# Kernel optimization log

Measured on AMD Instinct MI355X. Metric: run time of the kernel, lower is better.

## Reference

```python
import jax, jax.numpy as jnp
import numpy as np

# irreps kept in the output (sorted): 0e (dim 1), 1o (dim 3), 2e (dim 5)
IRS = (("0e", 1), ("1o", 3), ("2e", 5))
# multiplicity of each irrep in the reduced symmetric tensor product basis per order
MULS = {1: {"0e": 1, "1o": 1, "2e": 1},
        2: {"0e": 2, "1o": 2, "2e": 3},
        3: {"0e": 4, "1o": 6, "2e": 8}}
N, C, D, S, CORR = 1024, 128, 9, 10, 3  # nodes, channels, irreps dim (0e+1o+2e), species, correlation


def setup_inputs() -> dict:
    key = jax.random.key(0)
    ks = iter(jax.random.split(key, 64))
    inp = {"x": jax.random.normal(next(ks), (N, C, D), dtype=jnp.float32)}
    for order in range(1, CORR + 1):
        for ir, idim in IRS:
            mul = MULS[order][ir]
            # U basis tensor: shape (D,)*order + (mul, ir_dim); CG-like tensors are sparse
            u = jax.random.normal(next(ks), (D,) * order + (mul, idim), dtype=jnp.float32)
            mask = jax.random.bernoulli(next(ks), 0.25, u.shape)
            inp[f"u{order}_{ir}"] = jnp.where(mask, u, 0.0)
            # per-species weights, stddev mul**-0.5 ('element' gradient normalization)
            inp[f"w{order}_{ir}"] = jax.random.normal(next(ks), (S, mul, C), dtype=jnp.float32) * (mul ** -0.5)
    inp["index"] = jax.random.randint(next(ks), (N,), 0, S)
    return inp


def _forward(x, index, us, ws):
    # x: (N, C, D) node features; index: (N,) species ids
    out = {}
    for order in range(CORR, 0, -1):
        for ir, idim in IRS:
            w = ws[order][ir][index]  # per-species weight gather -> (N, mul, C)
            u = us[order][ir]          # (D,)*order + (mul, idim)
            if order == CORR:
                # highest order: contract one D axis with x together with the weights
                out[ir] = jnp.einsum('...jki,zkc,zcj->zc...i', u, w, x)
            else:
                # accumulate this order's term, then contract one more D axis with x
                acc = out[ir] + jnp.einsum('...ki,zkc->zc...i', u, w)
                out[ir] = jnp.einsum('zc...ji,zcj->zc...i', acc, x)
    # final out[ir]: (N, C, idim); axis_to_mul -> concat of (N, C*idim) blocks
    return jnp.concatenate([out[ir].reshape(N, C * idim) for ir, idim in IRS], axis=-1)


def reference(x, u1_0e, u1_1o, u1_2e, u2_0e, u2_1o, u2_2e, u3_0e, u3_1o, u3_2e,
              w1_0e, w1_1o, w1_2e, w2_0e, w2_1o, w2_2e, w3_0e, w3_1o, w3_2e, index):
    us = {1: {"0e": u1_0e, "1o": u1_1o, "2e": u1_2e},
          2: {"0e": u2_0e, "1o": u2_1o, "2e": u2_2e},
          3: {"0e": u3_0e, "1o": u3_1o, "2e": u3_2e}}
    ws = {1: {"0e": w1_0e, "1o": w1_1o, "2e": w1_2e},
          2: {"0e": w2_0e, "1o": w2_1o, "2e": w2_2e},
          3: {"0e": w3_0e, "1o": w3_1o, "2e": w3_2e}}
    return _forward(x, index, us, ws)
```

## Files before the change

kernel.cpp:

```cpp
#include <hip/hip_runtime.h>


#define NMONO3 165
#define NMONO2 45
#define NMONO  219
#define NN 1024
#define NC 128
#define NS 10
#define NPB 2
#define MAXBLK (NN / NPB + NS)

__device__ __forceinline__ void decode3(int m, int& A, int& B, int& J) {
    int cnt = 0;
    for (int a = 0; a < 9; a++)
        for (int b = a; b < 9; b++)
            for (int j = b; j < 9; j++) {
                if (cnt == m) { A = a; B = b; J = j; return; }
                cnt++;
            }
}
__device__ __forceinline__ void decode2(int m, int& A, int& B) {
    int cnt = 0;
    for (int a = 0; a < 9; a++)
        for (int b = a; b < 9; b++) {
            if (cnt == m) { A = a; B = b; return; }
            cnt++;
        }
}

__global__ __launch_bounds__(128) void precompute_uw(
    const float* __restrict__ u1_0e, const float* __restrict__ w1_0e,
    const float* __restrict__ u1_1o, const float* __restrict__ w1_1o,
    const float* __restrict__ u1_2e, const float* __restrict__ w1_2e,
    const float* __restrict__ u2_0e, const float* __restrict__ w2_0e,
    const float* __restrict__ u2_1o, const float* __restrict__ w2_1o,
    const float* __restrict__ u2_2e, const float* __restrict__ w2_2e,
    const float* __restrict__ u3_0e, const float* __restrict__ w3_0e,
    const float* __restrict__ u3_1o, const float* __restrict__ w3_1o,
    const float* __restrict__ u3_2e, const float* __restrict__ w3_2e,
    float* __restrict__ uwA, float* __restrict__ uwB)
{
    const int blk  = blockIdx.x;
    const int s    = blk / NMONO;
    const int mono = blk % NMONO;
    const int c    = threadIdx.x;
    const int t    = threadIdx.x;
    __shared__ float usum[64];

    if (mono < NMONO3) {
        if (t < 62) {
            int A, B, J; decode3(mono, A, B, J);
            const float* u; int mul, idim, k, i;
            if (t < 4)       { u = u3_0e; mul = 4; idim = 1; k = t; i = 0; }
            else if (t < 22) { u = u3_1o; mul = 6; idim = 3; int r = t - 4;  k = r / 3; i = r % 3; }
            else             { u = u3_2e; mul = 8; idim = 5; int r = t - 22; k = r / 5; i = r % 5; }
            int arr[6] = { A*81+B*9+J, A*81+J*9+B, B*81+A*9+J, B*81+J*9+A, J*81+A*9+B, J*81+B*9+A };
            float sv = 0.f;
            for (int p = 0; p < 6; p++) {
                bool dup = false;
                for (int q = 0; q < p; q++) if (arr[q] == arr[p]) dup = true;
                if (!dup) sv += u[arr[p]*(mul*idim) + k*idim + i];
            }
            usum[t] = sv;
        }
    } else if (mono < NMONO3 + NMONO2) {
        if (t < 23) {
            int A, B; decode2(mono - NMONO3, A, B);
            const float* u; int mul, idim, k, i;
            if (t < 2)      { u = u2_0e; mul = 2; idim = 1; k = t; i = 0; }
            else if (t < 8) { u = u2_1o; mul = 2; idim = 3; int r = t - 2; k = r / 3; i = r % 3; }
            else            { u = u2_2e; mul = 3; idim = 5; int r = t - 8; k = r / 5; i = r % 5; }
            float sv = u[(A*9+B)*(mul*idim) + k*idim + i];
            if (A != B) sv += u[(B*9+A)*(mul*idim) + k*idim + i];
            usum[t] = sv;
        }
    } else {
        if (t < 9) {
            int A = mono - (NMONO3 + NMONO2);
            float sv;
            if (t == 0)      sv = u1_0e[A];
            else if (t < 4)  sv = u1_1o[A*3 + (t-1)];
            else             sv = u1_2e[A*5 + (t-4)];
            usum[t] = sv;
        }
    }
    __syncthreads();

    float o[9];
    if (mono < NMONO3) {
        float v = 0.f;
        #pragma unroll
        for (int k = 0; k < 4; k++) v += usum[k] * w3_0e[(s*4+k)*NC + c];
        o[0] = v;
        #pragma unroll
        for (int i = 0; i < 3; i++) {
            v = 0.f;
            #pragma unroll
            for (int k = 0; k < 6; k++) v += usum[4 + k*3 + i] * w3_1o[(s*6+k)*NC + c];
            o[1+i] = v;
        }
        #pragma unroll
        for (int i = 0; i < 5; i++) {
            v = 0.f;
            #pragma unroll
            for (int k = 0; k < 8; k++) v += usum[22 + k*5 + i] * w3_2e[(s*8+k)*NC + c];
            o[4+i] = v;
        }
    } else if (mono < NMONO3 + NMONO2) {
        float v = 0.f;
        #pragma unroll
        for (int k = 0; k < 2; k++) v += usum[k] * w2_0e[(s*2+k)*NC + c];
        o[0] = v;
        #pragma unroll
        for (int i = 0; i < 3; i++) {
            v = 0.f;
            #pragma unroll
            for (int k = 0; k < 2; k++) v += usum[2 + k*3 + i] * w2_1o[(s*2+k)*NC + c];
            o[1+i] = v;
        }
        #pragma unroll
        for (int i = 0; i < 5; i++) {
            v = 0.f;
            #pragma unroll
            for (int k = 0; k < 3; k++) v += usum[8 + k*5 + i] * w2_2e[(s*3+k)*NC + c];
            o[4+i] = v;
        }
    } else {
        o[0] = usum[0] * w1_0e[s*NC + c];
        #pragma unroll
        for (int i = 0; i < 3; i++) o[1+i] = usum[1+i] * w1_1o[s*NC + c];
        #pragma unroll
        for (int i = 0; i < 5; i++) o[4+i] = usum[4+i] * w1_2e[s*NC + c];
    }

    const size_t base = (size_t)(s*NMONO + mono)*NC + c;
    #pragma unroll
    for (int q = 0; q < 8; q++) uwA[base*8 + q] = o[q];
    uwB[base] = o[8];
}

__global__ __launch_bounds__(1024) void build_groups(
    const int* __restrict__ index,
    int* __restrict__ perm,
    int* __restrict__ offs,
    int* __restrict__ blockmap)
{
    __shared__ int cnt[NS], pos[NS];
    const int t = threadIdx.x;
    if (t < NS) cnt[t] = 0;
    __syncthreads();
    const int s = index[t];
    atomicAdd(&cnt[s], 1);
    __syncthreads();
    if (t == 0) {
        int o = 0;
        for (int i = 0; i < NS; i++) { offs[i] = o; pos[i] = o; o += cnt[i]; }
        offs[NS] = o;
        int b = 0;
        for (int i = 0; i < NS; i++) {
            int nb = (cnt[i] + NPB - 1) / NPB;
            for (int j = 0; j < nb; j++) { blockmap[2*b] = i; blockmap[2*b+1] = j; b++; }
        }
        for (; b < MAXBLK; b++) { blockmap[2*b] = -1; blockmap[2*b+1] = 0; }
    }
    __syncthreads();
    const int r = atomicAdd(&pos[s], 1);
    perm[r] = t;
}

__global__ __launch_bounds__(256) void symcon_main(
    const float* __restrict__ x,
    const int* __restrict__ perm, const int* __restrict__ offs,
    const int* __restrict__ blockmap,
    const float* __restrict__ uwA, const float* __restrict__ uwB,
    float* __restrict__ out)
{
    __shared__ float lx[256][11];
    __shared__ int   abj[NMONO];

    const int tid = threadIdx.x;
    const int c   = tid & 127;
    const int h   = tid >> 7;

    if (tid < NMONO) {
        int a, b, j;
        if (tid < NMONO3)               { decode3(tid, a, b, j); }
        else if (tid < NMONO3 + NMONO2) { decode2(tid - NMONO3, a, b); j = 9; }
        else                            { a = tid - (NMONO3 + NMONO2); b = 9; j = 9; }
        abj[tid] = (a << 8) | (b << 4) | j;
    }

    const int s     = blockmap[2*blockIdx.x];
    const int chunk = blockmap[2*blockIdx.x + 1];
    if (s < 0) return;
    const int gbeg = offs[s], gend = offs[s+1];
    const int pidx = gbeg + chunk*NPB + h;
    const bool valid = (pidx < gend);
    const int node = perm[valid ? pidx : gbeg];

    {
        const float* xp = x + ((size_t)node*NC + c)*9;
        #pragma unroll
        for (int d = 0; d < 9; d++) lx[tid][d] = xp[d];
        lx[tid][9] = 1.0f;
    }
    __syncthreads();

    float acc[9];
    #pragma unroll
    for (int q = 0; q < 9; q++) acc[q] = 0.f;

    const float* pA = uwA + ((size_t)s*NMONO*NC + c) * 8;
    const float* pB = uwB +  (size_t)s*NMONO*NC + c;
    const float* myx = &lx[tid][0];

    #pragma unroll 3
    for (int m = 0; m < NMONO; m++) {
        const int e = abj[m];
        const float pa = myx[(e >> 8) & 15];
        const float pb = myx[(e >> 4) & 15];
        const float pj = myx[e & 15];
        const float p  = pa * pb * pj;
        const float4 f0 = *(const float4*)(pA);
        const float4 f1 = *(const float4*)(pA + 4);
        const float  fb = *pB;
        acc[0] += f0.x*p; acc[1] += f0.y*p; acc[2] += f0.z*p; acc[3] += f0.w*p;
        acc[4] += f1.x*p; acc[5] += f1.y*p; acc[6] += f1.z*p; acc[7] += f1.w*p;
        acc[8] += fb*p;
        pA += NC*8; pB += NC;
    }

    if (valid) {
        float* orow = out + (size_t)node * 1152;
        orow[c] = acc[0];
        #pragma unroll
        for (int i = 0; i < 3; i++) orow[128 + c*3 + i] = acc[1+i];
        #pragma unroll
        for (int i = 0; i < 5; i++) orow[512 + c*5 + i] = acc[4+i];
    }
}

extern "C" void kernel_launch(void* const* d_in, const int* in_sizes, int n_in,
                              void* d_out, int out_size, void* d_ws, size_t ws_size,
                              hipStream_t stream)
{
    const float* x     = (const float*)d_in[0];
    const float* u1_0e = (const float*)d_in[1];
    const float* w1_0e = (const float*)d_in[2];
    const float* u1_1o = (const float*)d_in[3];
    const float* w1_1o = (const float*)d_in[4];
    const float* u1_2e = (const float*)d_in[5];
    const float* w1_2e = (const float*)d_in[6];
    const float* u2_0e = (const float*)d_in[7];
    const float* w2_0e = (const float*)d_in[8];
    const float* u2_1o = (const float*)d_in[9];
    const float* w2_1o = (const float*)d_in[10];
    const float* u2_2e = (const float*)d_in[11];
    const float* w2_2e = (const float*)d_in[12];
    const float* u3_0e = (const float*)d_in[13];
    const float* w3_0e = (const float*)d_in[14];
    const float* u3_1o = (const float*)d_in[15];
    const float* w3_1o = (const float*)d_in[16];
    const float* u3_2e = (const float*)d_in[17];
    const float* w3_2e = (const float*)d_in[18];
    const int*   index = (const int*)d_in[19];
    float* out = (float*)d_out;

    float* uwA = (float*)d_ws;
    float* uwB = uwA + (size_t)NS*NMONO*NC*8;
    int*   perm     = (int*)(uwB + (size_t)NS*NMONO*NC);
    int*   offs     = perm + NN;
    int*   blockmap = offs + (NS+1);

    hipLaunchKernelGGL(build_groups, dim3(1), dim3(NN), 0, stream,
        index, perm, offs, blockmap);

    hipLaunchKernelGGL(precompute_uw, dim3(NS*NMONO), dim3(128), 0, stream,
        u1_0e, w1_0e, u1_1o, w1_1o, u1_2e, w1_2e,
        u2_0e, w2_0e, u2_1o, w2_1o, u2_2e, w2_2e,
        u3_0e, w3_0e, u3_1o, w3_1o, u3_2e, w3_2e, uwA, uwB);

    hipLaunchKernelGGL(symcon_main, dim3(MAXBLK), dim3(256), 0, stream,
        x, perm, offs, blockmap, uwA, uwB, out);
}
```

Measured before the change: 168.6 us.

## Split monomial loop across four warps-groups with shared-memory reduction and XCD-aware block order

```diff
diff --git a/kernel.cpp b/kernel.cpp
--- a/kernel.cpp
+++ b/kernel.cpp
@@ -1,32 +1,46 @@
 #include <hip/hip_runtime.h>
 
 
-#define NMONO3 165
-#define NMONO2 45
-#define NMONO  219
+#define NMONO 219
+#define NPAIR 54
 #define NN 1024
 #define NC 128
 #define NS 10
 #define NPB 2
-#define MAXBLK (NN / NPB + NS)
-
-__device__ __forceinline__ void decode3(int m, int& A, int& B, int& J) {
-    int cnt = 0;
+#define PADBLK 528
+
+struct Tables {
+    int mt[NMONO];
+    int pair_ab[NPAIR];
+    int pair_m0[NPAIR + 1];
+    int qs[5];
+};
+
+constexpr Tables make_tables() {
+    Tables T{};
+    int m = 0, pg = 0;
     for (int a = 0; a < 9; a++)
-        for (int b = a; b < 9; b++)
-            for (int j = b; j < 9; j++) {
-                if (cnt == m) { A = a; B = b; J = j; return; }
-                cnt++;
-            }
-}
-__device__ __forceinline__ void decode2(int m, int& A, int& B) {
-    int cnt = 0;
-    for (int a = 0; a < 9; a++)
-        for (int b = a; b < 9; b++) {
-            if (cnt == m) { A = a; B = b; return; }
-            cnt++;
-        }
-}
+        for (int b = a; b < 10; b++) {
+            T.pair_ab[pg] = (a << 4) | b;
+            T.pair_m0[pg] = m;
+            for (int j = b; j < 10; j++) { T.mt[m] = (a << 8) | (b << 4) | j; m++; }
+            pg++;
+        }
+    T.pair_m0[NPAIR] = m;
+    T.qs[0] = 0; T.qs[4] = NPAIR;
+    for (int q = 1; q < 4; q++) {
+        int best = 0; long bestd = 1L << 40;
+        for (int p = 0; p <= NPAIR; p++) {
+            long d = 4L * T.pair_m0[p] - 219L * q;
+            if (d < 0) d = -d;
+            if (d < bestd) { bestd = d; best = p; }
+        }
+        T.qs[q] = best;
+    }
+    return T;
+}
+
+__device__ __constant__ const Tables TBL = make_tables();
 
 __global__ __launch_bounds__(128) void precompute_uw(
     const float* __restrict__ u1_0e, const float* __restrict__ w1_0e,
@@ -47,9 +61,13 @@
     const int t    = threadIdx.x;
     __shared__ float usum[64];
 
-    if (mono < NMONO3) {
+    const int e = TBL.mt[mono];
+    const int A = (e >> 8) & 15, B = (e >> 4) & 15, J = e & 15;
+    const bool deg3 = (J < 9);
+    const bool deg1 = (B == 9);
+
+    if (deg3) {
         if (t < 62) {
-            int A, B, J; decode3(mono, A, B, J);
             const float* u; int mul, idim, k, i;
             if (t < 4)       { u = u3_0e; mul = 4; idim = 1; k = t; i = 0; }
             else if (t < 22) { u = u3_1o; mul = 6; idim = 3; int r = t - 4;  k = r / 3; i = r % 3; }
@@ -63,9 +81,8 @@
             }
             usum[t] = sv;
         }
-    } else if (mono < NMONO3 + NMONO2) {
+    } else if (!deg1) {
         if (t < 23) {
-            int A, B; decode2(mono - NMONO3, A, B);
             const float* u; int mul, idim, k, i;
             if (t < 2)      { u = u2_0e; mul = 2; idim = 1; k = t; i = 0; }
             else if (t < 8) { u = u2_1o; mul = 2; idim = 3; int r = t - 2; k = r / 3; i = r % 3; }
@@ -76,7 +93,6 @@
         }
     } else {
         if (t < 9) {
-            int A = mono - (NMONO3 + NMONO2);
             float sv;
             if (t == 0)      sv = u1_0e[A];
             else if (t < 4)  sv = u1_1o[A*3 + (t-1)];
@@ -87,7 +103,7 @@
     __syncthreads();
 
     float o[9];
-    if (mono < NMONO3) {
+    if (deg3) {
         float v = 0.f;
         #pragma unroll
         for (int k = 0; k < 4; k++) v += usum[k] * w3_0e[(s*4+k)*NC + c];
@@ -106,7 +122,7 @@
             for (int k = 0; k < 8; k++) v += usum[22 + k*5 + i] * w3_2e[(s*8+k)*NC + c];
             o[4+i] = v;
         }
-    } else if (mono < NMONO3 + NMONO2) {
+    } else if (!deg1) {
         float v = 0.f;
         #pragma unroll
         for (int k = 0; k < 2; k++) v += usum[k] * w2_0e[(s*2+k)*NC + c];
@@ -134,8 +150,10 @@
     }
 
     const size_t base = (size_t)(s*NMONO + mono)*NC + c;
-    #pragma unroll
-    for (int q = 0; q < 8; q++) uwA[base*8 + q] = o[q];
+    float4 lo; lo.x = o[0]; lo.y = o[1]; lo.z = o[2]; lo.w = o[3];
+    float4 hi; hi.x = o[4]; hi.y = o[5]; hi.z = o[6]; hi.w = o[7];
+    *(float4*)(uwA + base*8)     = lo;
+    *(float4*)(uwA + base*8 + 4) = hi;
     uwB[base] = o[8];
 }
 
@@ -145,7 +163,8 @@
     int* __restrict__ offs,
     int* __restrict__ blockmap)
 {
-    __shared__ int cnt[NS], pos[NS];
+    __shared__ int cnt[NS], pos[NS], nbstart[NS+1];
+    __shared__ int sh_nch;
     const int t = threadIdx.x;
     if (t < NS) cnt[t] = 0;
     __syncthreads();
@@ -153,22 +172,37 @@
     atomicAdd(&cnt[s], 1);
     __syncthreads();
     if (t == 0) {
-        int o = 0;
-        for (int i = 0; i < NS; i++) { offs[i] = o; pos[i] = o; o += cnt[i]; }
-        offs[NS] = o;
-        int b = 0;
+        int o = 0, g = 0;
         for (int i = 0; i < NS; i++) {
-            int nb = (cnt[i] + NPB - 1) / NPB;
-            for (int j = 0; j < nb; j++) { blockmap[2*b] = i; blockmap[2*b+1] = j; b++; }
-        }
-        for (; b < MAXBLK; b++) { blockmap[2*b] = -1; blockmap[2*b+1] = 0; }
-    }
-    __syncthreads();
-    const int r = atomicAdd(&pos[s], 1);
-    perm[r] = t;
-}
-
-__global__ __launch_bounds__(256) void symcon_main(
+            offs[i] = o; pos[i] = o; o += cnt[i];
+            nbstart[i] = g; g += (cnt[i] + NPB - 1) / NPB;
+        }
+        offs[NS] = o; nbstart[NS] = g; sh_nch = g;
+    }
+    __syncthreads();
+    const int Nch = sh_nch;
+    for (int p = t; p < PADBLK; p += 1024) { blockmap[2*p] = -1; blockmap[2*p+1] = 0; }
+    __syncthreads();
+    if (t < Nch) {
+        const int g = t;
+        const int q = Nch >> 3, r = Nch & 7;
+        int x = 0, stx = 0;
+        for (int xx = 0; xx < 8; xx++) {
+            const int cx = q + (xx < r ? 1 : 0);
+            if (g < stx + cx) { x = xx; break; }
+            stx += cx;
+        }
+        const int p = x + 8 * (g - stx);
+        int sp = 0;
+        while (g >= nbstart[sp+1]) sp++;
+        blockmap[2*p]   = sp;
+        blockmap[2*p+1] = g - nbstart[sp];
+    }
+    const int r2 = atomicAdd(&pos[s], 1);
+    perm[r2] = t;
+}
+
+__global__ __launch_bounds__(1024, 8) void symcon_main(
     const float* __restrict__ x,
     const int* __restrict__ perm, const int* __restrict__ offs,
     const int* __restrict__ blockmap,
@@ -176,67 +210,76 @@
     float* __restrict__ out)
 {
     __shared__ float lx[256][11];
-    __shared__ int   abj[NMONO];
+    __shared__ float red[3][256][9];
 
     const int tid = threadIdx.x;
+    const int z   = tid >> 8;
+    const int hc  = tid & 255;
+    const int h   = hc >> 7;
     const int c   = tid & 127;
-    const int h   = tid >> 7;
-
-    if (tid < NMONO) {
-        int a, b, j;
-        if (tid < NMONO3)               { decode3(tid, a, b, j); }
-        else if (tid < NMONO3 + NMONO2) { decode2(tid - NMONO3, a, b); j = 9; }
-        else                            { a = tid - (NMONO3 + NMONO2); b = 9; j = 9; }
-        abj[tid] = (a << 8) | (b << 4) | j;
-    }
 
     const int s     = blockmap[2*blockIdx.x];
     const int chunk = blockmap[2*blockIdx.x + 1];
     if (s < 0) return;
     const int gbeg = offs[s], gend = offs[s+1];
-    const int pidx = gbeg + chunk*NPB + h;
-    const bool valid = (pidx < gend);
-    const int node = perm[valid ? pidx : gbeg];
-
-    {
-        const float* xp = x + ((size_t)node*NC + c)*9;
-        #pragma unroll
-        for (int d = 0; d < 9; d++) lx[tid][d] = xp[d];
-        lx[tid][9] = 1.0f;
-    }
-    __syncthreads();
+    const int p0   = gbeg + chunk*NPB;
+    const int node0 = perm[p0];
+    const bool v1   = (p0 + 1 < gend);
+    const int node1 = perm[v1 ? p0 + 1 : p0];
+
+    for (int f = tid; f < 1152; f += 1024) {
+        const int ch = f / 9;
+        const int d  = f - ch*9;
+        lx[ch][d]     = x[(size_t)node0*1152 + f];
+        lx[128+ch][d] = x[(size_t)node1*1152 + f];
+    }
+    if (tid < 256) lx[tid][9] = 1.0f;
+    __syncthreads();
+
+    const float* lxr = &lx[hc][0];
+    const int pg0 = TBL.qs[z], pg1 = TBL.qs[z+1];
+    const int m0  = TBL.pair_m0[pg0];
+    const float* pA = uwA + ((size_t)(s*NMONO + m0)*NC + c) * 8;
+    const float* pB = uwB +  (size_t)(s*NMONO + m0)*NC + c;
 
     float acc[9];
     #pragma unroll
-    for (int q = 0; q < 9; q++) acc[q] = 0.f;
-
-    const float* pA = uwA + ((size_t)s*NMONO*NC + c) * 8;
-    const float* pB = uwB +  (size_t)s*NMONO*NC + c;
-    const float* myx = &lx[tid][0];
-
-    #pragma unroll 3
-    for (int m = 0; m < NMONO; m++) {
-        const int e = abj[m];
-        const float pa = myx[(e >> 8) & 15];
-        const float pb = myx[(e >> 4) & 15];
-        const float pj = myx[e & 15];
-        const float p  = pa * pb * pj;
-        const float4 f0 = *(const float4*)(pA);
-        const float4 f1 = *(const float4*)(pA + 4);
-        const float  fb = *pB;
-        acc[0] += f0.x*p; acc[1] += f0.y*p; acc[2] += f0.z*p; acc[3] += f0.w*p;
-        acc[4] += f1.x*p; acc[5] += f1.y*p; acc[6] += f1.z*p; acc[7] += f1.w*p;
-        acc[8] += fb*p;
-        pA += NC*8; pB += NC;
-    }
-
-    if (valid) {
-        float* orow = out + (size_t)node * 1152;
-        orow[c] = acc[0];
-        #pragma unroll
-        for (int i = 0; i < 3; i++) orow[128 + c*3 + i] = acc[1+i];
-        #pragma unroll
-        for (int i = 0; i < 5; i++) orow[512 + c*5 + i] = acc[4+i];
+    for (int i = 0; i < 9; i++) acc[i] = 0.f;
+
+    for (int pg = pg0; pg < pg1; ++pg) {
+        const int ab = TBL.pair_ab[pg];
+        const int a = ab >> 4, b = ab & 15;
+        const float p2 = lxr[a] * lxr[b];
+        for (int j = b; j < 10; ++j) {
+            const float p  = p2 * lxr[j];
+            const float4 f0 = *(const float4*)(pA);
+            const float4 f1 = *(const float4*)(pA + 4);
+            const float  fb = *pB;
+            acc[0] += f0.x*p; acc[1] += f0.y*p; acc[2] += f0.z*p; acc[3] += f0.w*p;
+            acc[4] += f1.x*p; acc[5] += f1.y*p; acc[6] += f1.z*p; acc[7] += f1.w*p;
+            acc[8] += fb*p;
+            pA += NC*8; pB += NC;
+        }
+    }
+
+    if (z > 0) {
+        #pragma unroll
+        for (int i = 0; i < 9; i++) red[z-1][hc][i] = acc[i];
+    }
+    __syncthreads();
+    if (z == 0) {
+        #pragma unroll
+        for (int i = 0; i < 9; i++)
+            acc[i] += red[0][hc][i] + red[1][hc][i] + red[2][hc][i];
+        if (h == 0 || v1) {
+            const int node = h ? node1 : node0;
+            float* orow = out + (size_t)node * 1152;
+            orow[c] = acc[0];
+            #pragma unroll
+            for (int i = 0; i < 3; i++) orow[128 + c*3 + i] = acc[1+i];
+            #pragma unroll
+            for (int i = 0; i < 5; i++) orow[512 + c*5 + i] = acc[4+i];
+        }
     }
 }
 
@@ -280,6 +323,6 @@
         u2_0e, w2_0e, u2_1o, w2_1o, u2_2e, w2_2e,
         u3_0e, w3_0e, u3_1o, w3_1o, u3_2e, w3_2e, uwA, uwB);
 
-    hipLaunchKernelGGL(symcon_main, dim3(MAXBLK), dim3(256), 0, stream,
+    hipLaunchKernelGGL(symcon_main, dim3(PADBLK), dim3(1024), 0, stream,
         x, perm, offs, blockmap, uwA, uwB, out);
 }
```

Result: faster. 158.1 us (-6.2%).
